# Kernel tuning notes

Measured on AMD Instinct MI355X. Metric: run time of the kernel, lower is better.

The kernel has to match this reference:

```python
import jax, jax.numpy as jnp
import numpy as np

N, E, IN_DIM, OUT_DIM, EDGE_DIM = 50000, 800000, 256, 128, 64
NEG_SLOPE = 0.2


def setup_inputs() -> dict:
    key = jax.random.key(0)
    ks = jax.random.split(key, 8)
    xavier = lambda k, shape: jax.random.normal(k, shape, jnp.float32) * np.float32(np.sqrt(2.0 / (shape[0] + shape[1])))
    return {
        "nfeat": jax.random.normal(ks[0], (N, IN_DIM), jnp.float32),
        "ex": jax.random.normal(ks[1], (E, EDGE_DIM), jnp.float32),
        "src": jax.random.randint(ks[2], (E,), 0, N),
        "dst": jax.random.randint(ks[3], (E,), 0, N),
        "W_fc": xavier(ks[4], (OUT_DIM, IN_DIM)),
        "b_fc": jnp.zeros((OUT_DIM,), jnp.float32),
        "W_att": xavier(ks[5], (1, 2 * OUT_DIM + EDGE_DIM)),
        "b_att": jnp.zeros((1,), jnp.float32),
        "W_edge": xavier(ks[6], (OUT_DIM, EDGE_DIM)),
        "b_edge": jnp.zeros((OUT_DIM,), jnp.float32),
        "W_eatt": xavier(ks[7], (EDGE_DIM, EDGE_DIM)),
        "b_eatt": jnp.zeros((EDGE_DIM,), jnp.float32),
    }


def reference(nfeat, ex, src, dst, W_fc, b_fc, W_att, b_att, W_edge, b_edge, W_eatt, b_eatt):
    n = nfeat.shape[0]
    # node transform: z = fc(nfeat)  [N, OUT]
    z = nfeat @ W_fc.T + b_fc
    # edge transform for attention score calc  [E, EDGE_DIM]
    ex_t = ex @ W_eatt.T + b_eatt
    z_src = z[src]                                   # [E, OUT] gather
    # attention logits on concat[z_src, z_dst, ex_t]  [E, 1]
    z2 = jnp.concatenate([z_src, z[dst], ex_t], axis=1)
    e = jax.nn.leaky_relu(z2 @ W_att.T + b_att, NEG_SLOPE)
    # edge feature message  [E, OUT]
    ez = ex @ W_edge.T + b_edge
    # segment softmax over incoming edges of each dst node
    m = jax.ops.segment_max(e, dst, num_segments=n)  # [N, 1]
    w = jnp.exp(e - m[dst])
    denom = jax.ops.segment_sum(w, dst, num_segments=n)
    alpha = w / denom[dst]                           # [E, 1]
    # h = sum_e alpha * z_src + sum_e alpha * ez (apply_attention_on_edge)
    h = jax.ops.segment_sum(alpha * (z_src + ez), dst, num_segments=n)  # [N, OUT]
    return h, alpha
```

## Files before the change

kernel.cpp:

```cpp
#include <hip/hip_runtime.h>
#include <math.h>
#include <float.h>

#define IN_D 256
#define OUT_D 128
#define ED_D 64
#define NEG 0.2f

__global__ __launch_bounds__(256) void k_init(
        const float* __restrict__ W_att, const float* __restrict__ b_att,
        const float* __restrict__ W_eatt, const float* __restrict__ b_eatt,
        const float* __restrict__ W_fc, const float* __restrict__ W_edge,
        float* __restrict__ u, float* __restrict__ c0,
        float* __restrict__ Wt_fc, float2* __restrict__ Wt2,
        int* __restrict__ cnt, int* __restrict__ fill, int N) {
    int idx = blockIdx.x * 256 + threadIdx.x;
    if (idx < N) { cnt[idx] = 0; fill[idx] = 0; }
    if (idx < IN_D * OUT_D) {
        int k = idx >> 7, d = idx & 127;
        Wt_fc[idx] = W_fc[d * IN_D + k];
    }
    if (idx < ED_D * (OUT_D / 2)) {
        int k = idx >> 6, l = idx & 63;
        Wt2[idx] = make_float2(W_edge[(2 * l) * ED_D + k], W_edge[(2 * l + 1) * ED_D + k]);
    }
    if (idx < ED_D) {
        float acc = 0.f;
        for (int j = 0; j < ED_D; ++j) acc += W_att[256 + j] * W_eatt[j * ED_D + idx];
        u[idx] = acc;
    }
    if (idx == ED_D) {
        float c = 0.f;
        for (int j = 0; j < ED_D; ++j) c += W_att[256 + j] * b_eatt[j];
        c0[0] = c + b_att[0];
    }
}

__global__ __launch_bounds__(256) void k_hist(const int* __restrict__ dst,
                                              int* __restrict__ cnt, int E) {
    int i = blockIdx.x * 256 + threadIdx.x;
    if (i < E) atomicAdd(&cnt[dst[i]], 1);
}

__global__ __launch_bounds__(256) void k_node(
        const float* __restrict__ nfeat, const float* __restrict__ Wt_fc,
        const float* __restrict__ b_fc, const float* __restrict__ W_att,
        float* __restrict__ z, float* __restrict__ asrc, float* __restrict__ adst, int n) {
    __shared__ float sa[32][130];
    __shared__ float sb[32][128];
    int t = threadIdx.x;
    int tx = t & 15, ty = t >> 4;
    int row_base = blockIdx.x * 128;

    float acc[8][8];
#pragma unroll
    for (int i = 0; i < 8; ++i)
#pragma unroll
        for (int j = 0; j < 8; ++j) acc[i][j] = 0.f;

    int ar = t >> 3, af = t & 7;
    int bk = t >> 5, bn = t & 31;

    for (int k0 = 0; k0 < IN_D; k0 += 32) {
#pragma unroll
        for (int p = 0; p < 4; ++p) {
            int r = ar + p * 32;
            int node = row_base + r; if (node >= n) node = n - 1;
            float4 v = *(const float4*)(nfeat + (size_t)node * IN_D + k0 + af * 4);
            sa[af * 4 + 0][r] = v.x;
            sa[af * 4 + 1][r] = v.y;
            sa[af * 4 + 2][r] = v.z;
            sa[af * 4 + 3][r] = v.w;
        }
#pragma unroll
        for (int p = 0; p < 4; ++p) {
            int kk = bk + p * 8;
            float4 v = *(const float4*)(Wt_fc + (size_t)(k0 + kk) * 128 + bn * 4);
            *(float4*)&sb[kk][bn * 4] = v;
        }
        __syncthreads();
#pragma unroll 8
        for (int kk = 0; kk < 32; ++kk) {
            float a0[8], b0[8];
            *(float4*)&a0[0] = *(const float4*)&sa[kk][ty * 8];
            *(float4*)&a0[4] = *(const float4*)&sa[kk][ty * 8 + 4];
            *(float4*)&b0[0] = *(const float4*)&sb[kk][tx * 8];
            *(float4*)&b0[4] = *(const float4*)&sb[kk][tx * 8 + 4];
#pragma unroll
            for (int i = 0; i < 8; ++i)
#pragma unroll
                for (int j = 0; j < 8; ++j)
                    acc[i][j] = fmaf(a0[i], b0[j], acc[i][j]);
        }
        __syncthreads();
    }

    float w1v[8], w2v[8], bf[8];
#pragma unroll
    for (int j = 0; j < 8; ++j) {
        int nn = tx * 8 + j;
        w1v[j] = W_att[nn];
        w2v[j] = W_att[128 + nn];
        bf[j] = b_fc[nn];
    }
#pragma unroll
    for (int i = 0; i < 8; ++i) {
        int m = row_base + ty * 8 + i;
        bool ok = (m < n);
        float zv[8];
        float p1 = 0.f, p2 = 0.f;
#pragma unroll
        for (int j = 0; j < 8; ++j) {
            zv[j] = acc[i][j] + bf[j];
            p1 = fmaf(zv[j], w1v[j], p1);
            p2 = fmaf(zv[j], w2v[j], p2);
        }
#pragma unroll
        for (int off = 1; off <= 8; off <<= 1) {
            p1 += __shfl_xor(p1, off);
            p2 += __shfl_xor(p2, off);
        }
        if (ok) {
            float* zr = z + (size_t)m * OUT_D + tx * 8;
            *(float4*)zr = make_float4(zv[0], zv[1], zv[2], zv[3]);
            *(float4*)(zr + 4) = make_float4(zv[4], zv[5], zv[6], zv[7]);
            if (tx == 0) { asrc[m] = p1; adst[m] = p2; }
        }
    }
}

__global__ __launch_bounds__(1024) void k_scan(const int* __restrict__ cnt,
                                               int* __restrict__ rowptr, int N) {
    int t = threadIdx.x;
    int per = (N + 1023) / 1024;
    int b0 = t * per, b1 = b0 + per;
    if (b0 > N) b0 = N;
    if (b1 > N) b1 = N;
    int s = 0;
    for (int i = b0; i < b1; ++i) s += cnt[i];
    int wl = t & 63, w = t >> 6;
    int v = s;
#pragma unroll
    for (int off = 1; off < 64; off <<= 1) {
        int a = __shfl_up(v, off);
        if (wl >= off) v += a;
    }
    __shared__ int wsum[16], woff[16];
    if (wl == 63) wsum[w] = v;
    __syncthreads();
    if (t == 0) { int r = 0; for (int i = 0; i < 16; ++i) { woff[i] = r; r += wsum[i]; } }
    __syncthreads();
    int run = woff[w] + v - s;
    for (int i = b0; i < b1; ++i) { rowptr[i] = run; run += cnt[i]; }
    if (t == 1023) rowptr[N] = run;
}

__global__ __launch_bounds__(256) void k_edge(
        const float* __restrict__ ex, const int* __restrict__ src, const int* __restrict__ dst,
        const float* __restrict__ asrc, const float* __restrict__ adst,
        const float* __restrict__ u, const float* __restrict__ c0,
        const int* __restrict__ rowptr, int* __restrict__ fill,
        int4* __restrict__ csr, int E) {
    int i = blockIdx.x * 256 + threadIdx.x;
    if (i >= E) return;
    const float4* exr = (const float4*)(ex + (size_t)i * ED_D);
    const float4* u4 = (const float4*)u;
    float acc = 0.f;
#pragma unroll
    for (int q = 0; q < 16; ++q) {
        float4 a = exr[q], b = u4[q];
        acc += a.x * b.x + a.y * b.y + a.z * b.z + a.w * b.w;
    }
    int s = src[i], d = dst[i];
    float e = acc + asrc[s] + adst[d] + c0[0];
    e = (e > 0.f) ? e : NEG * e;
    int pos = rowptr[d] + atomicAdd(&fill[d], 1);
    csr[pos] = make_int4(__float_as_int(e), i, s, 0);
}

__global__ __launch_bounds__(256) void k_gather(
        const float2* __restrict__ zf2, const float* __restrict__ ex,
        const int4* __restrict__ csr, const int* __restrict__ rowptr,
        const float2* __restrict__ Wt2, const float* __restrict__ b_edge,
        float2* __restrict__ h2, float* __restrict__ alpha_out, int N) {
    __shared__ float2 swt[ED_D * 64];
    for (int i = threadIdx.x; i < ED_D * 64; i += 256) swt[i] = Wt2[i];
    __syncthreads();
    int lane = threadIdx.x & 63;
    int wid = blockIdx.x * 4 + (threadIdx.x >> 6);
    int nw = gridDim.x * 4;
    float2 be2 = ((const float2*)b_edge)[lane];
    for (int n = wid; n < N; n += nw) {
        int beg = rowptr[n], end = rowptr[n + 1];
        int deg = end - beg;
        if (deg == 0) {
            h2[(size_t)n * 64 + lane] = make_float2(0.f, 0.f);
            continue;
        }
        float2 accz = make_float2(0.f, 0.f);
        float accx = 0.f;
        if (deg <= 64) {
            int4 me = make_int4(0, 0, 0, 0);
            float lg = -FLT_MAX;
            if (lane < deg) { me = csr[beg + lane]; lg = __int_as_float(me.x); }
            float m = lg;
#pragma unroll
            for (int off = 32; off >= 1; off >>= 1) m = fmaxf(m, __shfl_xor(m, off));
            float wv = (lane < deg) ? expf(lg - m) : 0.f;
            float sw = wv;
#pragma unroll
            for (int off = 32; off >= 1; off >>= 1) sw += __shfl_xor(sw, off);
            float al = wv / sw;
            if (lane < deg) alpha_out[me.y] = al;
            int j = 0;
            for (; j + 8 <= deg; j += 8) {
                float a[8]; int s[8], e[8];
#pragma unroll
                for (int q = 0; q < 8; ++q) {
                    a[q] = __shfl(al, j + q);
                    s[q] = __shfl(me.z, j + q);
                    e[q] = __shfl(me.y, j + q);
                }
                float2 zv[8]; float xv[8];
#pragma unroll
                for (int q = 0; q < 8; ++q) {
                    zv[q] = zf2[(size_t)s[q] * 64 + lane];
                    xv[q] = ex[(size_t)e[q] * 64 + lane];
                }
#pragma unroll
                for (int q = 0; q < 8; ++q) {
                    accz.x = fmaf(a[q], zv[q].x, accz.x);
                    accz.y = fmaf(a[q], zv[q].y, accz.y);
                    accx = fmaf(a[q], xv[q], accx);
                }
            }
            for (; j + 4 <= deg; j += 4) {
                float a[4]; int s[4], e[4];
#pragma unroll
                for (int q = 0; q < 4; ++q) {
                    a[q] = __shfl(al, j + q);
                    s[q] = __shfl(me.z, j + q);
                    e[q] = __shfl(me.y, j + q);
                }
                float2 zv[4]; float xv[4];
#pragma unroll
                for (int q = 0; q < 4; ++q) {
                    zv[q] = zf2[(size_t)s[q] * 64 + lane];
                    xv[q] = ex[(size_t)e[q] * 64 + lane];
                }
#pragma unroll
                for (int q = 0; q < 4; ++q) {
                    accz.x = fmaf(a[q], zv[q].x, accz.x);
                    accz.y = fmaf(a[q], zv[q].y, accz.y);
                    accx = fmaf(a[q], xv[q], accx);
                }
            }
            for (; j < deg; ++j) {
                float aq = __shfl(al, j);
                int sq = __shfl(me.z, j), eq = __shfl(me.y, j);
                float2 zq = zf2[(size_t)sq * 64 + lane];
                float xq = ex[(size_t)eq * 64 + lane];
                accz.x = fmaf(aq, zq.x, accz.x);
                accz.y = fmaf(aq, zq.y, accz.y);
                accx = fmaf(aq, xq, accx);
            }
        } else {
            float m = -FLT_MAX;
            for (int c = beg + lane; c < end; c += 64)
                m = fmaxf(m, __int_as_float(csr[c].x));
#pragma unroll
            for (int off = 32; off >= 1; off >>= 1) m = fmaxf(m, __shfl_xor(m, off));
            float sw = 0.f;
            for (int c = beg + lane; c < end; c += 64)
                sw += expf(__int_as_float(csr[c].x) - m);
#pragma unroll
            for (int off = 32; off >= 1; off >>= 1) sw += __shfl_xor(sw, off);
            float rden = 1.f / sw;
            for (int c = beg; c < end; c += 64) {
                int mcnt = end - c;
                if (mcnt > 64) mcnt = 64;
                int4 me = make_int4(0, 0, 0, 0);
                float al = 0.f;
                if (lane < mcnt) {
                    me = csr[c + lane];
                    al = expf(__int_as_float(me.x) - m) * rden;
                    alpha_out[me.y] = al;
                }
                int j = 0;
                for (; j + 4 <= mcnt; j += 4) {
                    float a[4]; int s[4], e[4];
#pragma unroll
                    for (int q = 0; q < 4; ++q) {
                        a[q] = __shfl(al, j + q);
                        s[q] = __shfl(me.z, j + q);
                        e[q] = __shfl(me.y, j + q);
                    }
                    float2 zv[4]; float xv[4];
#pragma unroll
                    for (int q = 0; q < 4; ++q) {
                        zv[q] = zf2[(size_t)s[q] * 64 + lane];
                        xv[q] = ex[(size_t)e[q] * 64 + lane];
                    }
#pragma unroll
                    for (int q = 0; q < 4; ++q) {
                        accz.x = fmaf(a[q], zv[q].x, accz.x);
                        accz.y = fmaf(a[q], zv[q].y, accz.y);
                        accx = fmaf(a[q], xv[q], accx);
                    }
                }
                for (; j < mcnt; ++j) {
                    float aq = __shfl(al, j);
                    int sq = __shfl(me.z, j), eq = __shfl(me.y, j);
                    float2 zq = zf2[(size_t)sq * 64 + lane];
                    float xq = ex[(size_t)eq * 64 + lane];
                    accz.x = fmaf(aq, zq.x, accz.x);
                    accz.y = fmaf(aq, zq.y, accz.y);
                    accx = fmaf(aq, xq, accx);
                }
            }
        }
        float2 hv = make_float2(accz.x + be2.x, accz.y + be2.y);
#pragma unroll 8
        for (int k = 0; k < 64; ++k) {
            float a = __shfl(accx, k);
            float2 w2 = swt[k * 64 + lane];
            hv.x = fmaf(a, w2.x, hv.x);
            hv.y = fmaf(a, w2.y, hv.y);
        }
        h2[(size_t)n * 64 + lane] = hv;
    }
}

extern "C" void kernel_launch(void* const* d_in, const int* in_sizes, int n_in,
                              void* d_out, int out_size, void* d_ws, size_t ws_size,
                              hipStream_t stream) {
    const float* nfeat = (const float*)d_in[0];
    const float* ex    = (const float*)d_in[1];
    const int*   src   = (const int*)d_in[2];
    const int*   dst   = (const int*)d_in[3];
    const float* W_fc  = (const float*)d_in[4];
    const float* b_fc  = (const float*)d_in[5];
    const float* W_att = (const float*)d_in[6];
    const float* b_att = (const float*)d_in[7];
    const float* W_edge = (const float*)d_in[8];
    const float* b_edge = (const float*)d_in[9];
    const float* W_eatt = (const float*)d_in[10];
    const float* b_eatt = (const float*)d_in[11];
    int N = in_sizes[0] / IN_D;
    int E = in_sizes[2];

    float* h_out = (float*)d_out;
    float* alpha_out = h_out + (size_t)N * OUT_D;

    char* w = (char*)d_ws;
    auto alloc = [&](size_t bytes) { char* p = w; w += (bytes + 255) & ~255ull; return p; };
    float* z      = (float*)alloc((size_t)N * OUT_D * 4);
    float* asrc   = (float*)alloc((size_t)N * 4);
    float* adst   = (float*)alloc((size_t)N * 4);
    int* cnt      = (int*)alloc((size_t)N * 4);
    int* rowptr   = (int*)alloc(((size_t)N + 1) * 4);
    int* fill     = (int*)alloc((size_t)N * 4);
    int4* csr     = (int4*)alloc((size_t)E * 16);
    float* Wt_fc  = (float*)alloc((size_t)IN_D * OUT_D * 4);
    float2* Wt2   = (float2*)alloc((size_t)ED_D * 64 * 8);
    float* u      = (float*)alloc(64 * 4);
    float* c0     = (float*)alloc(4);

    int init_total = N > IN_D * OUT_D ? N : IN_D * OUT_D;
    k_init<<<(init_total + 255) / 256, 256, 0, stream>>>(
        W_att, b_att, W_eatt, b_eatt, W_fc, W_edge, u, c0, Wt_fc, Wt2, cnt, fill, N);
    k_hist<<<(E + 255) / 256, 256, 0, stream>>>(dst, cnt, E);
    k_node<<<(N + 127) / 128, 256, 0, stream>>>(nfeat, Wt_fc, b_fc, W_att, z, asrc, adst, N);
    k_scan<<<1, 1024, 0, stream>>>(cnt, rowptr, N);
    k_edge<<<(E + 255) / 256, 256, 0, stream>>>(ex, src, dst, asrc, adst, u, c0,
                                                rowptr, fill, csr, E);
    k_gather<<<(N + 3) / 4, 256, 0, stream>>>((const float2*)z, ex, csr, rowptr,
                                              (const float2*)Wt2, b_edge,
                                              (float2*)h_out, alpha_out, N);
}
```

Baseline: 430.5 us.

## Coalesce edge dot loads, half-wave gather with wider loads, split edge matmul kernel

k_edge now has each wave read 64 edge rows cooperatively, 16 lanes per row with float4 loads, and reduce each dot product with shuffles through shared memory. Before, each thread read its own row, so loads were strided. k_gather has each half-wave handle a different edge, using float4 z and float2 ex loads, and combines the halves with a cross-half shuffle. The W_edge projection of the aggregated ex moves to a new k_xmm kernel that reads an xsum buffer from the workspace. This adds one launch and a round trip of N×64 floats through global memory, and gather no longer has to load the weight table into shared memory.

```diff
diff --git a/kernel.cpp b/kernel.cpp
--- a/kernel.cpp
+++ b/kernel.cpp
@@ -161,168 +161,199 @@
         const float* __restrict__ u, const float* __restrict__ c0,
         const int* __restrict__ rowptr, int* __restrict__ fill,
         int4* __restrict__ csr, int E) {
-    int i = blockIdx.x * 256 + threadIdx.x;
-    if (i >= E) return;
-    const float4* exr = (const float4*)(ex + (size_t)i * ED_D);
-    const float4* u4 = (const float4*)u;
-    float acc = 0.f;
-#pragma unroll
-    for (int q = 0; q < 16; ++q) {
-        float4 a = exr[q], b = u4[q];
-        acc += a.x * b.x + a.y * b.y + a.z * b.z + a.w * b.w;
-    }
-    int s = src[i], d = dst[i];
-    float e = acc + asrc[s] + adst[d] + c0[0];
-    e = (e > 0.f) ? e : NEG * e;
-    int pos = rowptr[d] + atomicAdd(&fill[d], 1);
-    csr[pos] = make_int4(__float_as_int(e), i, s, 0);
+    __shared__ float sdot[4][64];
+    int lane = threadIdx.x & 63, wv = threadIdx.x >> 6;
+    int base = (blockIdx.x * 4 + wv) * 64;
+    if (base >= E) return;
+    float4 uu = ((const float4*)u)[lane & 15];
+    const float4* ex4 = (const float4*)ex;
+#pragma unroll 4
+    for (int r = 0; r < 16; ++r) {
+        int e = base + r * 4 + (lane >> 4);
+        float4 x = (e < E) ? ex4[(size_t)e * 16 + (lane & 15)]
+                           : make_float4(0.f, 0.f, 0.f, 0.f);
+        float d = x.x * uu.x + x.y * uu.y + x.z * uu.z + x.w * uu.w;
+        d += __shfl_xor(d, 1);
+        d += __shfl_xor(d, 2);
+        d += __shfl_xor(d, 4);
+        d += __shfl_xor(d, 8);
+        if ((lane & 15) == 0) sdot[wv][r * 4 + (lane >> 4)] = d;
+    }
+    int e = base + lane;
+    if (e < E) {
+        float acc = sdot[wv][lane];
+        int s = src[e], d = dst[e];
+        float lg = acc + asrc[s] + adst[d] + c0[0];
+        lg = (lg > 0.f) ? lg : NEG * lg;
+        int pos = rowptr[d] + atomicAdd(&fill[d], 1);
+        csr[pos] = make_int4(__float_as_int(lg), e, s, 0);
+    }
 }
 
 __global__ __launch_bounds__(256) void k_gather(
-        const float2* __restrict__ zf2, const float* __restrict__ ex,
+        const float4* __restrict__ zf4, const float2* __restrict__ ex2,
         const int4* __restrict__ csr, const int* __restrict__ rowptr,
+        float4* __restrict__ h4, float* __restrict__ alpha_out,
+        float2* __restrict__ xsum2, int N) {
+    int lane = threadIdx.x & 63;
+    int half = lane >> 5, hl = lane & 31;
+    int n = blockIdx.x * 4 + (threadIdx.x >> 6);
+    if (n >= N) return;
+    int beg = rowptr[n], end = rowptr[n + 1];
+    int deg = end - beg;
+    if (deg == 0) return;
+    float4 accz = make_float4(0.f, 0.f, 0.f, 0.f);
+    float2 accx = make_float2(0.f, 0.f);
+
+    if (deg <= 64) {
+        int4 me = make_int4(0, 0, 0, 0);
+        float lg = -FLT_MAX;
+        if (lane < deg) { me = csr[beg + lane]; lg = __int_as_float(me.x); }
+        float m = lg;
+#pragma unroll
+        for (int off = 32; off >= 1; off >>= 1) m = fmaxf(m, __shfl_xor(m, off));
+        float wvv = (lane < deg) ? expf(lg - m) : 0.f;
+        float sw = wvv;
+#pragma unroll
+        for (int off = 32; off >= 1; off >>= 1) sw += __shfl_xor(sw, off);
+        float al = wvv / sw;
+        if (lane < deg) alpha_out[me.y] = al;
+        int j = 0;
+        for (; j + 8 <= deg; j += 8) {
+            float a[4]; int s[4], e[4];
+#pragma unroll
+            for (int q = 0; q < 4; ++q) {
+                int idx = j + 2 * q + half;
+                a[q] = __shfl(al, idx);
+                s[q] = __shfl(me.z, idx);
+                e[q] = __shfl(me.y, idx);
+            }
+            float4 zv[4]; float2 xv[4];
+#pragma unroll
+            for (int q = 0; q < 4; ++q) {
+                zv[q] = zf4[(size_t)s[q] * 32 + hl];
+                xv[q] = ex2[(size_t)e[q] * 32 + hl];
+            }
+#pragma unroll
+            for (int q = 0; q < 4; ++q) {
+                accz.x = fmaf(a[q], zv[q].x, accz.x);
+                accz.y = fmaf(a[q], zv[q].y, accz.y);
+                accz.z = fmaf(a[q], zv[q].z, accz.z);
+                accz.w = fmaf(a[q], zv[q].w, accz.w);
+                accx.x = fmaf(a[q], xv[q].x, accx.x);
+                accx.y = fmaf(a[q], xv[q].y, accx.y);
+            }
+        }
+        for (; j < deg; j += 2) {
+            int idx = j + half;
+            float a = __shfl(al, idx);
+            int s = __shfl(me.z, idx), e = __shfl(me.y, idx);
+            float4 zv = zf4[(size_t)s * 32 + hl];
+            float2 xv = ex2[(size_t)e * 32 + hl];
+            accz.x = fmaf(a, zv.x, accz.x);
+            accz.y = fmaf(a, zv.y, accz.y);
+            accz.z = fmaf(a, zv.z, accz.z);
+            accz.w = fmaf(a, zv.w, accz.w);
+            accx.x = fmaf(a, xv.x, accx.x);
+            accx.y = fmaf(a, xv.y, accx.y);
+        }
+    } else {
+        float m = -FLT_MAX;
+        for (int c = beg + lane; c < end; c += 64)
+            m = fmaxf(m, __int_as_float(csr[c].x));
+#pragma unroll
+        for (int off = 32; off >= 1; off >>= 1) m = fmaxf(m, __shfl_xor(m, off));
+        float sw = 0.f;
+        for (int c = beg + lane; c < end; c += 64)
+            sw += expf(__int_as_float(csr[c].x) - m);
+#pragma unroll
+        for (int off = 32; off >= 1; off >>= 1) sw += __shfl_xor(sw, off);
+        float rden = 1.f / sw;
+        for (int c = beg; c < end; c += 64) {
+            int mcnt = end - c;
+            if (mcnt > 64) mcnt = 64;
+            int4 me = make_int4(0, 0, 0, 0);
+            float al = 0.f;
+            if (lane < mcnt) {
+                me = csr[c + lane];
+                al = expf(__int_as_float(me.x) - m) * rden;
+                alpha_out[me.y] = al;
+            }
+            int j = 0;
+            for (; j + 8 <= mcnt; j += 8) {
+                float a[4]; int s[4], e[4];
+#pragma unroll
+                for (int q = 0; q < 4; ++q) {
+                    int idx = j + 2 * q + half;
+                    a[q] = __shfl(al, idx);
+                    s[q] = __shfl(me.z, idx);
+                    e[q] = __shfl(me.y, idx);
+                }
+                float4 zv[4]; float2 xv[4];
+#pragma unroll
+                for (int q = 0; q < 4; ++q) {
+                    zv[q] = zf4[(size_t)s[q] * 32 + hl];
+                    xv[q] = ex2[(size_t)e[q] * 32 + hl];
+                }
+#pragma unroll
+                for (int q = 0; q < 4; ++q) {
+                    accz.x = fmaf(a[q], zv[q].x, accz.x);
+                    accz.y = fmaf(a[q], zv[q].y, accz.y);
+                    accz.z = fmaf(a[q], zv[q].z, accz.z);
+                    accz.w = fmaf(a[q], zv[q].w, accz.w);
+                    accx.x = fmaf(a[q], xv[q].x, accx.x);
+                    accx.y = fmaf(a[q], xv[q].y, accx.y);
+                }
+            }
+            for (; j < mcnt; j += 2) {
+                int idx = j + half;
+                float a = __shfl(al, idx);
+                int s = __shfl(me.z, idx), e = __shfl(me.y, idx);
+                float4 zv = zf4[(size_t)s * 32 + hl];
+                float2 xv = ex2[(size_t)e * 32 + hl];
+                accz.x = fmaf(a, zv.x, accz.x);
+                accz.y = fmaf(a, zv.y, accz.y);
+                accz.z = fmaf(a, zv.z, accz.z);
+                accz.w = fmaf(a, zv.w, accz.w);
+                accx.x = fmaf(a, xv.x, accx.x);
+                accx.y = fmaf(a, xv.y, accx.y);
+            }
+        }
+    }
+    accz.x += __shfl_xor(accz.x, 32);
+    accz.y += __shfl_xor(accz.y, 32);
+    accz.z += __shfl_xor(accz.z, 32);
+    accz.w += __shfl_xor(accz.w, 32);
+    accx.x += __shfl_xor(accx.x, 32);
+    accx.y += __shfl_xor(accx.y, 32);
+    if (half == 0) {
+        h4[(size_t)n * 32 + hl] = accz;
+        xsum2[(size_t)n * 32 + hl] = accx;
+    }
+}
+
+__global__ __launch_bounds__(256) void k_xmm(
         const float2* __restrict__ Wt2, const float* __restrict__ b_edge,
-        float2* __restrict__ h2, float* __restrict__ alpha_out, int N) {
+        const float* __restrict__ xsum, const int* __restrict__ rowptr,
+        float2* __restrict__ h2, int N) {
     __shared__ float2 swt[ED_D * 64];
     for (int i = threadIdx.x; i < ED_D * 64; i += 256) swt[i] = Wt2[i];
     __syncthreads();
     int lane = threadIdx.x & 63;
-    int wid = blockIdx.x * 4 + (threadIdx.x >> 6);
-    int nw = gridDim.x * 4;
+    int wv = threadIdx.x >> 6;
     float2 be2 = ((const float2*)b_edge)[lane];
-    for (int n = wid; n < N; n += nw) {
-        int beg = rowptr[n], end = rowptr[n + 1];
-        int deg = end - beg;
+    for (int n = blockIdx.x * 4 + wv; n < N; n += gridDim.x * 4) {
+        int deg = rowptr[n + 1] - rowptr[n];
         if (deg == 0) {
             h2[(size_t)n * 64 + lane] = make_float2(0.f, 0.f);
             continue;
         }
-        float2 accz = make_float2(0.f, 0.f);
-        float accx = 0.f;
-        if (deg <= 64) {
-            int4 me = make_int4(0, 0, 0, 0);
-            float lg = -FLT_MAX;
-            if (lane < deg) { me = csr[beg + lane]; lg = __int_as_float(me.x); }
-            float m = lg;
-#pragma unroll
-            for (int off = 32; off >= 1; off >>= 1) m = fmaxf(m, __shfl_xor(m, off));
-            float wv = (lane < deg) ? expf(lg - m) : 0.f;
-            float sw = wv;
-#pragma unroll
-            for (int off = 32; off >= 1; off >>= 1) sw += __shfl_xor(sw, off);
-            float al = wv / sw;
-            if (lane < deg) alpha_out[me.y] = al;
-            int j = 0;
-            for (; j + 8 <= deg; j += 8) {
-                float a[8]; int s[8], e[8];
-#pragma unroll
-                for (int q = 0; q < 8; ++q) {
-                    a[q] = __shfl(al, j + q);
-                    s[q] = __shfl(me.z, j + q);
-                    e[q] = __shfl(me.y, j + q);
-                }
-                float2 zv[8]; float xv[8];
-#pragma unroll
-                for (int q = 0; q < 8; ++q) {
-                    zv[q] = zf2[(size_t)s[q] * 64 + lane];
-                    xv[q] = ex[(size_t)e[q] * 64 + lane];
-                }
-#pragma unroll
-                for (int q = 0; q < 8; ++q) {
-                    accz.x = fmaf(a[q], zv[q].x, accz.x);
-                    accz.y = fmaf(a[q], zv[q].y, accz.y);
-                    accx = fmaf(a[q], xv[q], accx);
-                }
-            }
-            for (; j + 4 <= deg; j += 4) {
-                float a[4]; int s[4], e[4];
-#pragma unroll
-                for (int q = 0; q < 4; ++q) {
-                    a[q] = __shfl(al, j + q);
-                    s[q] = __shfl(me.z, j + q);
-                    e[q] = __shfl(me.y, j + q);
-                }
-                float2 zv[4]; float xv[4];
-#pragma unroll
-                for (int q = 0; q < 4; ++q) {
-                    zv[q] = zf2[(size_t)s[q] * 64 + lane];
-                    xv[q] = ex[(size_t)e[q] * 64 + lane];
-                }
-#pragma unroll
-                for (int q = 0; q < 4; ++q) {
-                    accz.x = fmaf(a[q], zv[q].x, accz.x);
-                    accz.y = fmaf(a[q], zv[q].y, accz.y);
-                    accx = fmaf(a[q], xv[q], accx);
-                }
-            }
-            for (; j < deg; ++j) {
-                float aq = __shfl(al, j);
-                int sq = __shfl(me.z, j), eq = __shfl(me.y, j);
-                float2 zq = zf2[(size_t)sq * 64 + lane];
-                float xq = ex[(size_t)eq * 64 + lane];
-                accz.x = fmaf(aq, zq.x, accz.x);
-                accz.y = fmaf(aq, zq.y, accz.y);
-                accx = fmaf(aq, xq, accx);
-            }
-        } else {
-            float m = -FLT_MAX;
-            for (int c = beg + lane; c < end; c += 64)
-                m = fmaxf(m, __int_as_float(csr[c].x));
-#pragma unroll
-            for (int off = 32; off >= 1; off >>= 1) m = fmaxf(m, __shfl_xor(m, off));
-            float sw = 0.f;
-            for (int c = beg + lane; c < end; c += 64)
-                sw += expf(__int_as_float(csr[c].x) - m);
-#pragma unroll
-            for (int off = 32; off >= 1; off >>= 1) sw += __shfl_xor(sw, off);
-            float rden = 1.f / sw;
-            for (int c = beg; c < end; c += 64) {
-                int mcnt = end - c;
-                if (mcnt > 64) mcnt = 64;
-                int4 me = make_int4(0, 0, 0, 0);
-                float al = 0.f;
-                if (lane < mcnt) {
-                    me = csr[c + lane];
-                    al = expf(__int_as_float(me.x) - m) * rden;
-                    alpha_out[me.y] = al;
-                }
-                int j = 0;
-                for (; j + 4 <= mcnt; j += 4) {
-                    float a[4]; int s[4], e[4];
-#pragma unroll
-                    for (int q = 0; q < 4; ++q) {
-                        a[q] = __shfl(al, j + q);
-                        s[q] = __shfl(me.z, j + q);
-                        e[q] = __shfl(me.y, j + q);
-                    }
-                    float2 zv[4]; float xv[4];
-#pragma unroll
-                    for (int q = 0; q < 4; ++q) {
-                        zv[q] = zf2[(size_t)s[q] * 64 + lane];
-                        xv[q] = ex[(size_t)e[q] * 64 + lane];
-                    }
-#pragma unroll
-                    for (int q = 0; q < 4; ++q) {
-                        accz.x = fmaf(a[q], zv[q].x, accz.x);
-                        accz.y = fmaf(a[q], zv[q].y, accz.y);
-                        accx = fmaf(a[q], xv[q], accx);
-                    }
-                }
-                for (; j < mcnt; ++j) {
-                    float aq = __shfl(al, j);
-                    int sq = __shfl(me.z, j), eq = __shfl(me.y, j);
-                    float2 zq = zf2[(size_t)sq * 64 + lane];
-                    float xq = ex[(size_t)eq * 64 + lane];
-                    accz.x = fmaf(aq, zq.x, accz.x);
-                    accz.y = fmaf(aq, zq.y, accz.y);
-                    accx = fmaf(aq, xq, accx);
-                }
-            }
-        }
-        float2 hv = make_float2(accz.x + be2.x, accz.y + be2.y);
+        float xk = xsum[(size_t)n * 64 + lane];
+        float2 hv = h2[(size_t)n * 64 + lane];
+        hv.x += be2.x; hv.y += be2.y;
 #pragma unroll 8
         for (int k = 0; k < 64; ++k) {
-            float a = __shfl(accx, k);
+            float a = __shfl(xk, k);
             float2 w2 = swt[k * 64 + lane];
             hv.x = fmaf(a, w2.x, hv.x);
             hv.y = fmaf(a, w2.y, hv.y);
@@ -361,6 +392,7 @@
     int* rowptr   = (int*)alloc(((size_t)N + 1) * 4);
     int* fill     = (int*)alloc((size_t)N * 4);
     int4* csr     = (int4*)alloc((size_t)E * 16);
+    float* xsum   = (float*)alloc((size_t)N * ED_D * 4);
     float* Wt_fc  = (float*)alloc((size_t)IN_D * OUT_D * 4);
     float2* Wt2   = (float2*)alloc((size_t)ED_D * 64 * 8);
     float* u      = (float*)alloc(64 * 4);
@@ -374,7 +406,8 @@
     k_scan<<<1, 1024, 0, stream>>>(cnt, rowptr, N);
     k_edge<<<(E + 255) / 256, 256, 0, stream>>>(ex, src, dst, asrc, adst, u, c0,
                                                 rowptr, fill, csr, E);
-    k_gather<<<(N + 3) / 4, 256, 0, stream>>>((const float2*)z, ex, csr, rowptr,
-                                              (const float2*)Wt2, b_edge,
-                                              (float2*)h_out, alpha_out, N);
-}
+    k_gather<<<(N + 3) / 4, 256, 0, stream>>>((const float4*)z, (const float2*)ex, csr, rowptr,
+                                              (float4*)h_out, alpha_out, (float2*)xsum, N);
+    k_xmm<<<(N + 3) / 4, 256, 0, stream>>>((const float2*)Wt2, b_edge, xsum, rowptr,
+                                           (float2*)h_out, N);
+}
```

Result: no change. 433.0 us (+0.6%).
